# Performance work log

Hardware: AMD Instinct MI355X
Metric: run time of the kernel (lower is better)

The kernel has to match this reference:

```python
import jax, jax.numpy as jnp
import numpy as np

B, L, D, H = 4, 2048, 256, 512


def silu_backward(x):
    s = jax.nn.silu(x)
    return s + jax.nn.sigmoid(x) * (1.0 - s)


def setup_inputs() -> dict:
    key = jax.random.key(0)
    ks = jax.random.split(key, 12)
    sc = 0.02
    return {
        "x": jax.random.normal(ks[0], (B, L, D), jnp.float32),
        "W1": jax.random.normal(ks[1], (B, H, D), jnp.float32) * sc,
        "W2": jax.random.normal(ks[2], (B, D, H), jnp.float32) * sc,
        "Wq": jax.random.normal(ks[3], (D, D), jnp.float32) * sc,
        "bq": jnp.zeros((D,), jnp.float32),
        "Wk": jax.random.normal(ks[4], (D, D), jnp.float32) * sc,
        "bk": jnp.zeros((D,), jnp.float32),
        "Wv": jax.random.normal(ks[5], (D, D), jnp.float32) * sc,
        "bv": jnp.zeros((D,), jnp.float32),
        "w_lr": jax.random.normal(ks[6], (D,), jnp.float32) * sc,
        "b_lr": jnp.zeros((), jnp.float32),
        "w_wd": jax.random.normal(ks[7], (D,), jnp.float32) * sc,
        "b_wd": jnp.zeros((), jnp.float32),
        "log_base_lr": jnp.asarray(np.log(0.1), jnp.float32),
        "log_base_wd": jnp.asarray(np.log(0.5), jnp.float32),
    }


def reference(x, W1, W2, Wq, bq, Wk, bk, Wv, bv, w_lr, b_lr, w_wd, b_wd, log_base_lr, log_base_wd):
    b, l, d = x.shape
    query = x @ Wq + bq
    key = x @ Wk + bk
    value = x @ Wv + bv
    lr = jnp.exp(log_base_lr) * jax.nn.sigmoid(x @ w_lr + b_lr)          # [b,l]
    log_wd = jnp.log(1.0 - jnp.exp(log_base_wd) * jax.nn.sigmoid(x @ w_wd + b_wd))  # [b,l]

    wd_cross = jnp.exp(jnp.cumsum(log_wd, axis=1))                       # [b,l]
    idx = jnp.arange(l)
    strict_upper = idx[:, None] < idx[None, :]                           # (m, j): j > m
    A = jnp.where(strict_upper[None], log_wd[:, None, :], 0.0)           # [b,m,j]
    wd_inner = jnp.exp(jnp.cumsum(A, axis=2)) * (idx[:, None] <= idx[None, :])[None]  # [b,m,j]

    X1 = key
    Z1 = jnp.einsum('bhd,bld->blh', W1, X1)
    X2 = jax.nn.silu(Z1)
    Z2 = jnp.einsum('bdh,blh->bld', W2, X2)
    grad_Z2 = Z2 - value
    grad_X2 = jnp.einsum('bdh,bld->blh', W2, grad_Z2)
    grad_Z1 = silu_backward(Z1) * grad_X2

    X1_ = query
    mask_X1X1_ = jnp.einsum('bld,bmd->blm', X1, X1_) * wd_inner
    Z1_inner = -jnp.einsum('blh,bl,blm->bmh', grad_Z1, lr, mask_X1X1_)
    Z1_cross = jnp.einsum('bhd,bld,bl->blh', W1, X1_, wd_cross)
    Z1_ = Z1_inner + Z1_cross

    W1_next = (-jnp.einsum('blh,bl,bld->bhd', grad_Z1, lr * wd_inner[:, :, -1], X1)
               + W1 * wd_cross[:, -1][:, None, None])

    X2_ = jax.nn.silu(Z1_)
    mask_X2X2_ = jnp.einsum('blh,bmh->blm', X2, X2_) * wd_inner
    Z2_inner = -jnp.einsum('bld,bl,blm->bmd', grad_Z2, lr, mask_X2X2_)
    Z2_cross = jnp.einsum('bdh,blh,bl->bld', W2, X2_, wd_cross)
    Z2_ = Z2_inner + Z2_cross

    W2_next = (-jnp.einsum('bld,bl,blh->bdh', grad_Z2, lr * wd_inner[:, :, -1], X2)
               + W2 * wd_cross[:, -1][:, None, None])

    return (Z2_, W1_next, W2_next)
```

## Files before the change

### kernel.cpp

```cpp
#include <hip/hip_runtime.h>

typedef __bf16 bf16;
typedef __bf16 bf16x8 __attribute__((ext_vector_type(8)));
typedef __bf16 bf16x4 __attribute__((ext_vector_type(4)));
typedef float  f32x4  __attribute__((ext_vector_type(4)));

#define SB 72
#define SP 136
#define CUTOFF -25.0

__device__ __forceinline__ float silu_f(float x){
  float s = 1.f/(1.f+__expf(-x));
  return x*s;
}
__device__ __forceinline__ float silu_bwd_f(float x){
  float s = 1.f/(1.f+__expf(-x));
  float si = x*s;
  return si + s*(1.f-si);
}

struct MArgs {
  const bf16* A; const bf16* B;
  long sA, sB;
  int lda, ldb;
  int M, N, K;
  int mode;
  float* Cf; long sCf;
  bf16*  Cb; long sCb;
  bf16*  Cb2; long sCb2;
  bf16*  Ct;  long sCt;  int ldct;
  int ldc;
  const float* auxf; int ldax; long sAuxf;
  const bf16*  auxb; long sAuxb;
  const float* rowv; long sRowv;
  const double* cd;  long sCd;
  const float* ks;   long sKs;
  const float* clp;  long sClp;
  bf16* Q; bf16* Ko; float* Vo; const float* bqkv;
};

template<int TM>
__device__ __forceinline__ void gemm_body(const MArgs& g, int bm, int bn, int bz)
{
  const int row0 = bm*TM, col0 = bn*64;
  constexpr int NI  = TM/32;
  constexpr int TPR = 256/TM;
  constexpr int EPR = 64/TPR;
  constexpr int NCH = EPR/8;

  const bf16* A = g.A + (long)bz*g.sA;
  const bf16* B = g.B + (long)bz*g.sB;
  const float* ksp = g.ks ? g.ks + (long)bz*g.sKs : (const float*)0;
  const double* cd = g.cd ? g.cd + (long)bz*g.sCd : (const double*)0;
  float* Cf = g.Cf ? g.Cf + (long)bz*g.sCf : (float*)0;
  bf16* Cb  = g.Cb ? g.Cb + (long)bz*g.sCb : (bf16*)0;
  bf16* Cb2 = g.Cb2 ? g.Cb2 + (long)bz*g.sCb2 : (bf16*)0;
  bf16* Ct  = g.Ct ? g.Ct + (long)bz*g.sCt : (bf16*)0;
  const float* auxf = g.auxf ? g.auxf + (long)bz*g.sAuxf : (const float*)0;
  const bf16*  auxb = g.auxb ? g.auxb + (long)bz*g.sAuxb : (const bf16*)0;
  const float* rowv = g.rowv ? g.rowv + (long)bz*g.sRowv : (const float*)0;

  const int tid = threadIdx.x;
  const int mode = g.mode;
  const int lane = tid & 63;
  const int w = tid >> 6;
  const int wr = (w >> 1) * (TM/2), wc = (w & 1) * 32;
  const int l15 = lane & 15;
  const int quad = lane >> 4;

  __shared__ __align__(16) bf16 As[TM*SB];
  __shared__ __align__(16) bf16 Bs[64*SB];

  f32x4 acc[NI][2];
  #pragma unroll
  for (int i=0;i<NI;i++)
    #pragma unroll
    for (int j=0;j<2;j++)
      #pragma unroll
      for (int r=0;r<4;r++) acc[i][j][r] = 0.f;

  const int rowA = tid / TPR, kA = (tid % TPR) * EPR;
  const int rowB = tid >> 2,  kB = (tid & 3) * 16;

  int klo = 0;
  if (cd && ksp) {
    const double cref = cd[g.K-1];
    while (klo + 64 < g.K && (cref - cd[klo+63]) < CUTOFF) klo += 64;
  }

  for (int k0 = klo; k0 < g.K; k0 += 64) {
    {
      const bf16* s = A + (long)(row0+rowA)*g.lda + k0 + kA;
      bf16x8 v[NCH];
      #pragma unroll
      for (int p=0;p<NCH;p++) v[p] = *(const bf16x8*)(s + p*8);
      if (ksp) {
        #pragma unroll
        for (int p=0;p<NCH;p++)
          #pragma unroll
          for (int i=0;i<8;i++)
            v[p][i] = (bf16)((float)v[p][i] * ksp[k0+kA+p*8+i]);
      }
      #pragma unroll
      for (int p=0;p<NCH;p++) *(bf16x8*)&As[rowA*SB + kA + p*8] = v[p];
    }
    {
      const bf16* s = B + (long)(col0+rowB)*g.ldb + k0 + kB;
      *(bf16x8*)&Bs[rowB*SB + kB]     = *(const bf16x8*)s;
      *(bf16x8*)&Bs[rowB*SB + kB + 8] = *(const bf16x8*)(s+8);
    }
    __syncthreads();
    #pragma unroll
    for (int ch=0; ch<2; ch++){
      bf16x8 af[NI], bf2[2];
      #pragma unroll
      for (int i=0;i<NI;i++) af[i]  = *(const bf16x8*)&As[(wr + i*16 + l15)*SB + ch*32 + quad*8];
      #pragma unroll
      for (int j=0;j<2;j++) bf2[j] = *(const bf16x8*)&Bs[(wc + j*16 + l15)*SB + ch*32 + quad*8];
      #pragma unroll
      for (int i=0;i<NI;i++)
        #pragma unroll
        for (int j=0;j<2;j++)
          acc[i][j] = __builtin_amdgcn_mfma_f32_16x16x32_bf16(af[i], bf2[j], acc[i][j], 0, 0, 0);
    }
    __syncthreads();
  }

  float clv = 0.f;
  if (mode == 10) clv = *(g.clp + (long)bz*g.sClp);

  #pragma unroll
  for (int i=0;i<NI;i++){
    const int rb = row0 + wr + i*16 + quad*4;
    #pragma unroll
    for (int j=0;j<2;j++){
      const int c = col0 + wc + j*16 + l15;
      bf16 tv[4]; bool doT = false;
      #pragma unroll
      for (int reg=0; reg<4; reg++){
        const int r = rb + reg;
        float v = acc[i][j][reg];
        const long co = (long)r*g.ldc + c;
        switch (mode) {
          case 1: {
            Cb[co]  = (bf16)v;
            bf16 sv = (bf16)silu_f(v);
            Cb2[co] = sv;
            tv[reg] = sv; doT = true;
          } break;
          case 2: {
            bf16 o = (bf16)(v - auxf[(long)r*g.ldax + c]);
            Cb[co] = o; tv[reg] = o; doT = true;
          } break;
          case 3: {
            bf16 o = (bf16)(silu_bwd_f((float)auxb[(long)r*g.ldax + c]) * v * rowv[r]);
            Cb[co] = o; tv[reg] = o; doT = true;
          } break;
          case 10: {
            Cf[co] = v + auxf[(long)r*g.ldax + c]*clv;
          } break;
          case 11: {
            float o = v + g.bqkv[c];
            if (c < 256)      g.Q [(long)r*256 + c]       = (bf16)o;
            else if (c < 512) { g.Ko[(long)r*256 + (c-256)] = (bf16)o; tv[reg] = (bf16)o; doT = true; }
            else              g.Vo[(long)r*256 + (c-512)] = o;
          } break;
        }
      }
      if (doT && Ct) {
        bf16x4 t4 = { tv[0], tv[1], tv[2], tv[3] };
        if (mode == 11) {
          const int b = rb / g.ldct, l = rb % g.ldct;
          *(bf16x4*)&Ct[(long)b*g.sCt + (long)(c-256)*g.ldct + l] = t4;
        } else {
          *(bf16x4*)&Ct[(long)c*g.ldct + rb] = t4;
        }
      }
    }
  }
}

__global__ __launch_bounds__(256)
void mfma_gemm128(MArgs g){ gemm_body<128>(g, blockIdx.x, blockIdx.y, blockIdx.z); }

__global__ __launch_bounds__(256)
void mfma_gemm64(MArgs g){ gemm_body<64>(g, blockIdx.x, blockIdx.y, blockIdx.z); }

__global__ __launch_bounds__(256)
void wnext_gemm(MArgs g1, MArgs g2){
  const int z = blockIdx.z;
  const MArgs& g = (z < 4) ? g1 : g2;
  const int bz = z & 3;
  if ((int)blockIdx.x*128 >= g.M || (int)blockIdx.y*64 >= g.N) return;
  gemm_body<128>(g, blockIdx.x, blockIdx.y, bz);
}

struct FArgs {
  const bf16 *A, *B1, *B2, *W;
  long sA, sB1, sB2, sW;
  int ldb2;
  const double* cd; long sCd;
  const float* colv; long sColv;
  const float* wdc; long sWdc;
  float* Cf; long sCf;
  bf16* Cb; long sCb;
  int ldc;
};

template<int KS64, int ISF2, int ZSPLIT>
__global__ __launch_bounds__(256)
void fused_inner(FArgs g)
{
  const int m0 = blockIdx.x*64, n0 = blockIdx.y*128;
  const int bz   = ZSPLIT ? (blockIdx.z >> 1) : blockIdx.z;
  const int half = ZSPLIT ? (blockIdx.z & 1)  : 0;
  const int K1 = KS64*64;
  const bf16* A  = g.A  + (long)bz*g.sA;
  const bf16* B1 = g.B1 + (long)bz*g.sB1;
  const bf16* B2 = g.B2 + (long)bz*g.sB2;
  const bf16* W  = g.W  + (long)bz*g.sW;
  const double* cd = g.cd + (long)bz*g.sCd;
  const float* colv = ISF2 ? (g.colv + (long)bz*g.sColv) : (const float*)0;
  const float* wdc = g.wdc + (long)bz*g.sWdc;

  int lb = 0;
  while (lb + 128 <= m0 && (cd[m0] - cd[lb+127]) < CUTOFF) lb += 128;
  if (ZSPLIT && half == 1 && lb + 128 > m0) return;

  const int tid = threadIdx.x;
  const int lane = tid & 63, w = tid >> 6;
  const int wr = (w>>1)*32, wc = (w&1)*64;
  const int l15 = lane & 15, quad = lane >> 4;
  const int rowA = tid >> 2, kA = (tid & 3) * 16;
  const int rowB = tid >> 1, kB = (tid & 1) * 32;

  __shared__ __align__(16) bf16 As[64*SB];
  __shared__ __align__(16) bf16 Bs[128*SB];
  __shared__ __align__(16) bf16 Ps[64*SP];

  f32x4 O[2][4];
  #pragma unroll
  for (int i=0;i<2;i++)
    #pragma unroll
    for (int j=0;j<4;j++)
      #pragma unroll
      for (int r=0;r<4;r++) O[i][j][r] = 0.f;

  if (half == 0) {
    for (int ks=0; ks<KS64; ks++){
      const int k0 = ks*64;
      {
        const bf16* s = A + (long)(m0+rowA)*K1 + k0 + kA;
        *(bf16x8*)&As[rowA*SB + kA]     = *(const bf16x8*)s;
        *(bf16x8*)&As[rowA*SB + kA + 8] = *(const bf16x8*)(s+8);
      }
      {
        const bf16* s = W + (long)(n0+rowB)*K1 + k0 + kB;
        #pragma unroll
        for (int p=0;p<4;p++) *(bf16x8*)&Bs[rowB*SB + kB + p*8] = *(const bf16x8*)(s + p*8);
      }
      __syncthreads();
      #pragma unroll
      for (int ch=0; ch<2; ch++){
        bf16x8 af[2], bfr[4];
        #pragma unroll
        for (int i=0;i<2;i++) af[i]  = *(const bf16x8*)&As[(wr + i*16 + l15)*SB + ch*32 + quad*8];
        #pragma unroll
        for (int j=0;j<4;j++) bfr[j] = *(const bf16x8*)&Bs[(wc + j*16 + l15)*SB + ch*32 + quad*8];
        #pragma unroll
        for (int i=0;i<2;i++)
          #pragma unroll
          for (int j=0;j<4;j++)
            O[i][j] = __builtin_amdgcn_mfma_f32_16x16x32_bf16(af[i], bfr[j], O[i][j], 0, 0, 0);
      }
      __syncthreads();
    }
    #pragma unroll
    for (int i=0;i<2;i++)
      #pragma unroll
      for (int reg=0; reg<4; reg++){
        const float s = wdc[m0 + wr + i*16 + quad*4 + reg];
        #pragma unroll
        for (int j=0;j<4;j++) O[i][j][reg] *= s;
      }
  }

  const int lstep = ZSPLIT ? 256 : 128;
  for (int l0 = lb + half*128; l0 <= m0; l0 += lstep) {
    f32x4 P[2][4];
    #pragma unroll
    for (int i=0;i<2;i++)
      #pragma unroll
      for (int j=0;j<4;j++)
        #pragma unroll
        for (int r=0;r<4;r++) P[i][j][r] = 0.f;

    for (int ks=0; ks<KS64; ks++){
      const int k0 = ks*64;
      {
        const bf16* s = A + (long)(m0+rowA)*K1 + k0 + kA;
        *(bf16x8*)&As[rowA*SB + kA]     = *(const bf16x8*)s;
        *(bf16x8*)&As[rowA*SB + kA + 8] = *(const bf16x8*)(s+8);
      }
      {
        const bf16* s = B1 + (long)(l0+rowB)*K1 + k0 + kB;
        #pragma unroll
        for (int p=0;p<4;p++) *(bf16x8*)&Bs[rowB*SB + kB + p*8] = *(const bf16x8*)(s + p*8);
      }
      __syncthreads();
      #pragma unroll
      for (int ch=0; ch<2; ch++){
        bf16x8 af[2], bfr[4];
        #pragma unroll
        for (int i=0;i<2;i++) af[i]  = *(const bf16x8*)&As[(wr + i*16 + l15)*SB + ch*32 + quad*8];
        #pragma unroll
        for (int j=0;j<4;j++) bfr[j] = *(const bf16x8*)&Bs[(wc + j*16 + l15)*SB + ch*32 + quad*8];
        #pragma unroll
        for (int i=0;i<2;i++)
          #pragma unroll
          for (int j=0;j<4;j++)
            P[i][j] = __builtin_amdgcn_mfma_f32_16x16x32_bf16(af[i], bfr[j], P[i][j], 0, 0, 0);
      }
      __syncthreads();
    }

    {
      float cl[4], lrv[4];
      #pragma unroll
      for (int j=0;j<4;j++){
        const int l = l0 + wc + j*16 + l15;
        cl[j] = (float)cd[l];
        if (ISF2) lrv[j] = colv[l];
      }
      #pragma unroll
      for (int i=0;i<2;i++)
        #pragma unroll
        for (int reg=0; reg<4; reg++){
          const int mloc = wr + i*16 + quad*4 + reg;
          const int m = m0 + mloc;
          const float cm2 = (float)cd[m];
          #pragma unroll
          for (int j=0;j<4;j++){
            const int lloc = wc + j*16 + l15;
            const int l = l0 + lloc;
            float v = -P[i][j][reg] * __expf(cm2 - cl[j]);
            if (ISF2) v *= lrv[j];
            if (l > m) v = 0.f;
            Ps[mloc*SP + lloc] = (bf16)v;
          }
        }
    }
    __syncthreads();

    for (int st=0; st<2; st++){
      {
        const bf16* s = B2 + (long)(n0+rowB)*g.ldb2 + l0 + st*64 + kB;
        #pragma unroll
        for (int p=0;p<4;p++) *(bf16x8*)&Bs[rowB*SB + kB + p*8] = *(const bf16x8*)(s + p*8);
      }
      __syncthreads();
      #pragma unroll
      for (int ch=0; ch<2; ch++){
        bf16x8 af[2], bfr[4];
        #pragma unroll
        for (int i=0;i<2;i++) af[i]  = *(const bf16x8*)&Ps[(wr + i*16 + l15)*SP + st*64 + ch*32 + quad*8];
        #pragma unroll
        for (int j=0;j<4;j++) bfr[j] = *(const bf16x8*)&Bs[(wc + j*16 + l15)*SB + ch*32 + quad*8];
        #pragma unroll
        for (int i=0;i<2;i++)
          #pragma unroll
          for (int j=0;j<4;j++)
            O[i][j] = __builtin_amdgcn_mfma_f32_16x16x32_bf16(af[i], bfr[j], O[i][j], 0, 0, 0);
      }
      __syncthreads();
    }
  }

  #pragma unroll
  for (int i=0;i<2;i++){
    const int rb = m0 + wr + i*16 + quad*4;
    #pragma unroll
    for (int j=0;j<4;j++){
      const int c = n0 + wc + j*16 + l15;
      #pragma unroll
      for (int reg=0; reg<4; reg++){
        const long co = (long)(rb+reg)*g.ldc + c;
        if (ZSPLIT)     unsafeAtomicAdd(&g.Cf[(long)bz*g.sCf + co], O[i][j][reg]);
        else if (ISF2)  g.Cf[(long)bz*g.sCf + co] = O[i][j][reg];
        else            g.Cb[(long)bz*g.sCb + co] = (bf16)silu_f(O[i][j][reg]);
      }
    }
  }
}

__global__ __launch_bounds__(256)
void conv_multi(const float* __restrict__ a, bf16* __restrict__ oa, long na,
                const float* __restrict__ b, bf16* __restrict__ ob, long nb,
                const float* __restrict__ c, bf16* __restrict__ oc, long nc)
{
  const int job = blockIdx.y;
  const float* src = job==0 ? a : (job==1 ? b : c);
  bf16* dst       = job==0 ? oa : (job==1 ? ob : oc);
  const long n    = job==0 ? na : (job==1 ? nb : nc);
  long i = ((long)blockIdx.x*256 + threadIdx.x)*8;
  if (i >= n) return;
  float4 x = *(const float4*)&src[i];
  float4 y = *(const float4*)&src[i+4];
  bf16x8 o;
  o[0]=(bf16)x.x; o[1]=(bf16)x.y; o[2]=(bf16)x.z; o[3]=(bf16)x.w;
  o[4]=(bf16)y.x; o[5]=(bf16)y.y; o[6]=(bf16)y.z; o[7]=(bf16)y.w;
  *(bf16x8*)&dst[i] = o;
}

__global__ __launch_bounds__(256)
void transpose_qkv(const float* __restrict__ Wq, const float* __restrict__ Wk,
                   const float* __restrict__ Wv, bf16* __restrict__ out)
{
  __shared__ bf16 t[64][72];
  const int z = blockIdx.z;
  const float* ip = z==0 ? Wq : (z==1 ? Wk : Wv);
  bf16* op = out + (long)z*256*256;
  const int r0 = blockIdx.x*64, c0 = blockIdx.y*64;
  const int tid = threadIdx.x;
  const int lr_ = tid>>2, lc = (tid&3)*16;
  #pragma unroll
  for (int q=0;q<4;q++){
    float4 a = *(const float4*)&ip[(long)(r0+lr_)*256 + c0+lc + q*4];
    t[lr_][lc+q*4+0] = (bf16)a.x; t[lr_][lc+q*4+1] = (bf16)a.y;
    t[lr_][lc+q*4+2] = (bf16)a.z; t[lr_][lc+q*4+3] = (bf16)a.w;
  }
  __syncthreads();
  const int oc = tid>>2, orr = (tid&3)*16;
  bf16x8 u, v;
  #pragma unroll
  for (int i=0;i<8;i++){ u[i] = t[orr+i][oc]; v[i] = t[orr+8+i][oc]; }
  *(bf16x8*)&op[(long)(c0+oc)*256 + r0+orr]   = u;
  *(bf16x8*)&op[(long)(c0+oc)*256 + r0+orr+8] = v;
}

__global__ __launch_bounds__(256)
void transpose_f32_bf16(const float* __restrict__ in, bf16* __restrict__ out,
                        int R, int C, long sIn, long sOut)
{
  __shared__ bf16 t[64][72];
  const float* ip = in + (long)blockIdx.z*sIn;
  bf16* op = out + (long)blockIdx.z*sOut;
  const int r0 = blockIdx.x*64, c0 = blockIdx.y*64;
  const int tid = threadIdx.x;
  const int lr_ = tid>>2, lc = (tid&3)*16;
  #pragma unroll
  for (int q=0;q<4;q++){
    float4 a = *(const float4*)&ip[(long)(r0+lr_)*C + c0+lc + q*4];
    t[lr_][lc+q*4+0] = (bf16)a.x; t[lr_][lc+q*4+1] = (bf16)a.y;
    t[lr_][lc+q*4+2] = (bf16)a.z; t[lr_][lc+q*4+3] = (bf16)a.w;
  }
  __syncthreads();
  const int oc = tid>>2, orr = (tid&3)*16;
  bf16x8 u, v;
  #pragma unroll
  for (int i=0;i<8;i++){ u[i] = t[orr+i][oc]; v[i] = t[orr+8+i][oc]; }
  *(bf16x8*)&op[(long)(c0+oc)*R + r0+orr]   = u;
  *(bf16x8*)&op[(long)(c0+oc)*R + r0+orr+8] = v;
}

__global__ __launch_bounds__(256)
void scalar_proj_kernel(const float* __restrict__ x,
                        const float* __restrict__ wlr, const float* __restrict__ blr,
                        const float* __restrict__ wwd, const float* __restrict__ bwd,
                        const float* __restrict__ lbl, const float* __restrict__ lbw,
                        float* __restrict__ lr, float* __restrict__ lw)
{
  const int row  = blockIdx.x*4 + (threadIdx.x >> 6);
  const int lane = threadIdx.x & 63;
  const float4 a = ((const float4*)(x + (long)row*256))[lane];
  const float4 u = ((const float4*)wlr)[lane];
  const float4 w = ((const float4*)wwd)[lane];
  float d1 = a.x*u.x + a.y*u.y + a.z*u.z + a.w*u.w;
  float d2 = a.x*w.x + a.y*w.y + a.z*w.z + a.w*w.w;
  #pragma unroll
  for (int off=32; off; off>>=1) {
    d1 += __shfl_down(d1, off);
    d2 += __shfl_down(d2, off);
  }
  if (lane == 0) {
    float s1 = 1.f/(1.f+expf(-(d1 + blr[0])));
    lr[row] = expf(lbl[0]) * s1;
    float s2 = 1.f/(1.f+expf(-(d2 + bwd[0])));
    lw[row] = logf(1.f - expf(lbw[0]) * s2);
  }
}

__global__ __launch_bounds__(256)
void cumsum_kernel(const float* __restrict__ lw, const float* __restrict__ lr,
                   double* __restrict__ cd, float* __restrict__ wdc,
                   float* __restrict__ se1, float* __restrict__ se2, int L,
                   const float* __restrict__ bq, const float* __restrict__ bk,
                   const float* __restrict__ bv, float* __restrict__ bqkv)
{
  const int b = blockIdx.x;
  const int t = threadIdx.x;
  if (b == 4) {
    for (int i = t; i < 768; i += 256)
      bqkv[i] = (i<256) ? bq[i] : ((i<512) ? bk[i-256] : bv[i-512]);
    return;
  }
  const float* lwb = lw + (long)b*L;
  __shared__ double sum_s[256];
  double loc[8];
  double s = 0.0;
  #pragma unroll
  for (int i=0;i<8;i++){ s += (double)lwb[t*8+i]; loc[i] = s; }
  sum_s[t] = s;
  __syncthreads();
  for (int off=1; off<256; off<<=1){
    double v = 0.0;
    if (t >= off) v = sum_s[t-off];
    __syncthreads();
    sum_s[t] += v;
    __syncthreads();
  }
  const double prefix = (t > 0) ? sum_s[t-1] : 0.0;
  const double total  = sum_s[255];
  #pragma unroll
  for (int i=0;i<8;i++){
    double c = prefix + loc[i];
    long idx = (long)b*L + t*8 + i;
    cd[idx]  = c;
    wdc[idx] = (float)exp(c);
    double e = exp(total - c);
    se1[idx] = (float)(-e);
    se2[idx] = (float)(-e) * lr[idx];
  }
}

extern "C" void kernel_launch(void* const* d_in, const int* in_sizes, int n_in,
                              void* d_out, int out_size, void* d_ws, size_t ws_size,
                              hipStream_t stream)
{
  const int Bn = 4, L = 2048, D = 256, H = 512;
  const long LD = (long)L*D, LH = (long)L*H, HD = (long)H*D;

  const float* x   = (const float*)d_in[0];
  const float* W1  = (const float*)d_in[1];
  const float* W2  = (const float*)d_in[2];
  const float* Wq  = (const float*)d_in[3];
  const float* bq  = (const float*)d_in[4];
  const float* Wk  = (const float*)d_in[5];
  const float* bk  = (const float*)d_in[6];
  const float* Wv  = (const float*)d_in[7];
  const float* bv  = (const float*)d_in[8];
  const float* wlr = (const float*)d_in[9];
  const float* blr = (const float*)d_in[10];
  const float* wwd = (const float*)d_in[11];
  const float* bwd = (const float*)d_in[12];
  const float* lbl = (const float*)d_in[13];
  const float* lbw = (const float*)d_in[14];
  (void)in_sizes; (void)n_in; (void)out_size; (void)ws_size;

  float* out0 = (float*)d_out;
  float* out1 = out0 + (long)Bn*LD;
  float* out2 = out1 + (long)Bn*HD;

  char* wsp = (char*)d_ws;
  size_t off = 0;
  auto alloc = [&](size_t bytes)->void*{
    void* p = wsp + off; off += (bytes + 255) & ~(size_t)255; return p;
  };
  bf16* xb    = (bf16*)alloc((size_t)Bn*LD*2);
  bf16* Wqkvt = (bf16*)alloc((size_t)3*D*D*2);
  float* bqkv = (float*)alloc((size_t)3*D*4);
  bf16* W1b  = (bf16*)alloc((size_t)Bn*HD*2);
  bf16* W2b  = (bf16*)alloc((size_t)Bn*HD*2);
  bf16* W2t  = (bf16*)alloc((size_t)Bn*HD*2);
  bf16* Qb   = (bf16*)alloc((size_t)Bn*LD*2);
  bf16* Kb   = (bf16*)alloc((size_t)Bn*LD*2);
  bf16* Kt   = (bf16*)alloc((size_t)Bn*LD*2);
  float* Vf  = (float*)alloc((size_t)Bn*LD*4);
  bf16* Z1b  = (bf16*)alloc((size_t)Bn*LH*2);
  bf16* X2b  = (bf16*)alloc((size_t)Bn*LH*2);
  bf16* X2t  = (bf16*)alloc((size_t)Bn*LH*2);
  bf16* gZb  = (bf16*)alloc((size_t)Bn*LD*2);
  bf16* gZt  = (bf16*)alloc((size_t)Bn*LD*2);
  bf16* A1b  = (bf16*)alloc((size_t)Bn*LH*2);
  bf16* A1t  = (bf16*)alloc((size_t)Bn*LH*2);
  bf16* X2_b = (bf16*)alloc((size_t)Bn*LH*2);
  float* lrb = (float*)alloc((size_t)Bn*L*4);
  float* lwb = (float*)alloc((size_t)Bn*L*4);
  float* wdc = (float*)alloc((size_t)Bn*L*4);
  float* se1 = (float*)alloc((size_t)Bn*L*4);
  float* se2 = (float*)alloc((size_t)Bn*L*4);
  double* cdb = (double*)alloc((size_t)Bn*L*8);

  auto run128 = [&](const MArgs& g, int Z){
    dim3 grid(g.M/128, g.N/64, Z);
    mfma_gemm128<<<grid, 256, 0, stream>>>(g);
  };
  auto run64 = [&](const MArgs& g, int Z){
    dim3 grid(g.M/64, g.N/64, Z);
    mfma_gemm64<<<grid, 256, 0, stream>>>(g);
  };

  hipMemsetAsync(out0, 0, (size_t)Bn*LD*4, stream);

  conv_multi<<<dim3(1024,3), 256, 0, stream>>>(x, xb, Bn*LD, W1, W1b, Bn*HD, W2, W2b, Bn*HD);
  transpose_qkv<<<dim3(4,4,3), 256, 0, stream>>>(Wq, Wk, Wv, Wqkvt);
  transpose_f32_bf16<<<dim3(4,8,Bn), 256, 0, stream>>>(W2, W2t, D, H, HD, HD);
  scalar_proj_kernel<<<dim3(Bn*L/4), 256, 0, stream>>>(x, wlr, blr, wwd, bwd, lbl, lbw, lrb, lwb);
  cumsum_kernel<<<dim3(5), 256, 0, stream>>>(lwb, lrb, cdb, wdc, se1, se2, L, bq, bk, bv, bqkv);

  {
    MArgs g{}; g.A = xb; g.lda = D; g.B = Wqkvt; g.ldb = D;
    g.M = Bn*L; g.N = 3*D; g.K = D; g.mode = 11; g.ldc = 0;
    g.Q = Qb; g.Ko = Kb; g.Vo = Vf; g.bqkv = bqkv;
    g.Ct = Kt; g.sCt = LD; g.ldct = L;
    run128(g, 1);
  }
  {
    MArgs g{}; g.A = Kb; g.lda = D; g.sA = LD; g.B = W1b; g.ldb = D; g.sB = HD;
    g.M = L; g.N = H; g.K = D; g.mode = 1; g.ldc = H;
    g.Cb = Z1b; g.sCb = LH; g.Cb2 = X2b; g.sCb2 = LH;
    g.Ct = X2t; g.sCt = LH; g.ldct = L; run64(g, Bn);
  }
  {
    MArgs g{}; g.A = X2b; g.lda = H; g.sA = LH; g.B = W2b; g.ldb = H; g.sB = HD;
    g.M = L; g.N = D; g.K = H; g.mode = 2; g.ldc = D;
    g.auxf = Vf; g.ldax = D; g.sAuxf = LD; g.Cb = gZb; g.sCb = LD;
    g.Ct = gZt; g.sCt = LD; g.ldct = L; run64(g, Bn);
  }
  {
    MArgs g{}; g.A = gZb; g.lda = D; g.sA = LD; g.B = W2t; g.ldb = D; g.sB = HD;
    g.M = L; g.N = H; g.K = D; g.mode = 3; g.ldc = H;
    g.auxb = Z1b; g.ldax = H; g.sAuxb = LH; g.rowv = lrb; g.sRowv = L;
    g.Cb = A1b; g.sCb = LH;
    g.Ct = A1t; g.sCt = LH; g.ldct = L; run64(g, Bn);
  }
  {
    FArgs f{};
    f.A = Qb;  f.sA = LD;  f.B1 = Kb;  f.sB1 = LD;
    f.B2 = A1t; f.sB2 = LH; f.ldb2 = L;
    f.W = W1b; f.sW = HD;
    f.cd = cdb; f.sCd = L; f.wdc = wdc; f.sWdc = L;
    f.Cb = X2_b; f.sCb = LH; f.ldc = H;
    fused_inner<4,0,0><<<dim3(L/64, H/128, Bn), 256, 0, stream>>>(f);
  }
  {
    FArgs f{};
    f.A = X2_b; f.sA = LH; f.B1 = X2b; f.sB1 = LH;
    f.B2 = gZt; f.sB2 = LD; f.ldb2 = L;
    f.W = W2b; f.sW = HD;
    f.cd = cdb; f.sCd = L; f.colv = lrb; f.sColv = L; f.wdc = wdc; f.sWdc = L;
    f.Cf = out0; f.sCf = LD; f.ldc = D;
    fused_inner<8,1,1><<<dim3(L/64, D/128, Bn*2), 256, 0, stream>>>(f);
  }
  {
    MArgs g1{}; g1.A = A1t; g1.lda = L; g1.sA = LH; g1.B = Kt; g1.ldb = L; g1.sB = LD;
    g1.M = H; g1.N = D; g1.K = L; g1.mode = 10; g1.ldc = D;
    g1.ks = se1; g1.sKs = L; g1.cd = cdb; g1.sCd = L;
    g1.auxf = W1; g1.ldax = D; g1.sAuxf = HD; g1.clp = wdc + (L-1); g1.sClp = L;
    g1.Cf = out1; g1.sCf = HD;

    MArgs g2{}; g2.A = gZt; g2.lda = L; g2.sA = LD; g2.B = X2t; g2.ldb = L; g2.sB = LH;
    g2.M = D; g2.N = H; g2.K = L; g2.mode = 10; g2.ldc = H;
    g2.ks = se2; g2.sKs = L; g2.cd = cdb; g2.sCd = L;
    g2.auxf = W2; g2.ldax = H; g2.sAuxf = HD; g2.clp = wdc + (L-1); g2.sClp = L;
    g2.Cf = out2; g2.sCf = HD;

    wnext_gemm<<<dim3(4,8,8), 256, 0, stream>>>(g1, g2);
  }
}
```

Before: 251.0 us.

## Double K-tile depth to 128, swizzle fused-inner LDS, loosen decay cutoff, merge transposes

Raises the K step of the generic GEMM and the fused inner kernel from 64 to 128, so there are half as many barrier pairs per tile. In the fused kernel the padded LDS layout is replaced by an XOR swizzle, and the P@B2 stage now uses one 128-wide staging pass instead of two 64-wide ones. The decay cutoff for skipping negligible tiles is loosened from -25 to -18 so more K blocks are skipped, which adds approximation error. The two weight-transpose launches are merged into one kernel. LDS use per block grows, which may reduce occupancy.

```diff
diff --git a/kernel.cpp b/kernel.cpp
--- a/kernel.cpp
+++ b/kernel.cpp
@@ -5,9 +5,12 @@
 typedef __bf16 bf16x4 __attribute__((ext_vector_type(4)));
 typedef float  f32x4  __attribute__((ext_vector_type(4)));
 
-#define SB 72
-#define SP 136
-#define CUTOFF -25.0
+#define SB2 136
+#define CUTOFF -18.0
+
+__device__ __forceinline__ int swz(int r, int c){
+  return r*128 + ((((c>>3) ^ (r&15)) << 3) | (c & 7));
+}
 
 __device__ __forceinline__ float silu_f(float x){
   float s = 1.f/(1.f+__expf(-x));
@@ -44,8 +47,8 @@
 {
   const int row0 = bm*TM, col0 = bn*64;
   constexpr int NI  = TM/32;
-  constexpr int TPR = 256/TM;
-  constexpr int EPR = 64/TPR;
+  constexpr int TPR = 256/(TM);
+  constexpr int EPR = 128/TPR;
   constexpr int NCH = EPR/8;
 
   const bf16* A = g.A + (long)bz*g.sA;
@@ -68,8 +71,8 @@
   const int l15 = lane & 15;
   const int quad = lane >> 4;
 
-  __shared__ __align__(16) bf16 As[TM*SB];
-  __shared__ __align__(16) bf16 Bs[64*SB];
+  __shared__ __align__(16) bf16 As[TM*SB2];
+  __shared__ __align__(16) bf16 Bs[64*SB2];
 
   f32x4 acc[NI][2];
   #pragma unroll
@@ -80,15 +83,15 @@
       for (int r=0;r<4;r++) acc[i][j][r] = 0.f;
 
   const int rowA = tid / TPR, kA = (tid % TPR) * EPR;
-  const int rowB = tid >> 2,  kB = (tid & 3) * 16;
+  const int rowB = tid >> 2,  kB = (tid & 3) * 32;
 
   int klo = 0;
   if (cd && ksp) {
     const double cref = cd[g.K-1];
-    while (klo + 64 < g.K && (cref - cd[klo+63]) < CUTOFF) klo += 64;
-  }
-
-  for (int k0 = klo; k0 < g.K; k0 += 64) {
+    while (klo + 128 < g.K && (cref - cd[klo+127]) < CUTOFF) klo += 128;
+  }
+
+  for (int k0 = klo; k0 < g.K; k0 += 128) {
     {
       const bf16* s = A + (long)(row0+rowA)*g.lda + k0 + kA;
       bf16x8 v[NCH];
@@ -102,21 +105,21 @@
             v[p][i] = (bf16)((float)v[p][i] * ksp[k0+kA+p*8+i]);
       }
       #pragma unroll
-      for (int p=0;p<NCH;p++) *(bf16x8*)&As[rowA*SB + kA + p*8] = v[p];
+      for (int p=0;p<NCH;p++) *(bf16x8*)&As[rowA*SB2 + kA + p*8] = v[p];
     }
     {
       const bf16* s = B + (long)(col0+rowB)*g.ldb + k0 + kB;
-      *(bf16x8*)&Bs[rowB*SB + kB]     = *(const bf16x8*)s;
-      *(bf16x8*)&Bs[rowB*SB + kB + 8] = *(const bf16x8*)(s+8);
+      #pragma unroll
+      for (int p=0;p<4;p++) *(bf16x8*)&Bs[rowB*SB2 + kB + p*8] = *(const bf16x8*)(s + p*8);
     }
     __syncthreads();
     #pragma unroll
-    for (int ch=0; ch<2; ch++){
+    for (int ch=0; ch<4; ch++){
       bf16x8 af[NI], bf2[2];
       #pragma unroll
-      for (int i=0;i<NI;i++) af[i]  = *(const bf16x8*)&As[(wr + i*16 + l15)*SB + ch*32 + quad*8];
-      #pragma unroll
-      for (int j=0;j<2;j++) bf2[j] = *(const bf16x8*)&Bs[(wc + j*16 + l15)*SB + ch*32 + quad*8];
+      for (int i=0;i<NI;i++) af[i]  = *(const bf16x8*)&As[(wr + i*16 + l15)*SB2 + ch*32 + quad*8];
+      #pragma unroll
+      for (int j=0;j<2;j++) bf2[j] = *(const bf16x8*)&Bs[(wc + j*16 + l15)*SB2 + ch*32 + quad*8];
       #pragma unroll
       for (int i=0;i<NI;i++)
         #pragma unroll
@@ -207,14 +210,14 @@
   int ldc;
 };
 
-template<int KS64, int ISF2, int ZSPLIT>
+template<int KS128, int ISF2, int ZSPLIT>
 __global__ __launch_bounds__(256)
 void fused_inner(FArgs g)
 {
   const int m0 = blockIdx.x*64, n0 = blockIdx.y*128;
   const int bz   = ZSPLIT ? (blockIdx.z >> 1) : blockIdx.z;
   const int half = ZSPLIT ? (blockIdx.z & 1)  : 0;
-  const int K1 = KS64*64;
+  const int K1 = KS128*128;
   const bf16* A  = g.A  + (long)bz*g.sA;
   const bf16* B1 = g.B1 + (long)bz*g.sB1;
   const bf16* B2 = g.B2 + (long)bz*g.sB2;
@@ -231,12 +234,12 @@
   const int lane = tid & 63, w = tid >> 6;
   const int wr = (w>>1)*32, wc = (w&1)*64;
   const int l15 = lane & 15, quad = lane >> 4;
-  const int rowA = tid >> 2, kA = (tid & 3) * 16;
-  const int rowB = tid >> 1, kB = (tid & 1) * 32;
-
-  __shared__ __align__(16) bf16 As[64*SB];
-  __shared__ __align__(16) bf16 Bs[128*SB];
-  __shared__ __align__(16) bf16 Ps[64*SP];
+  const int rowA = tid >> 2, kA = (tid & 3) * 32;
+  const int rowB = tid >> 1, kB = (tid & 1) * 64;
+
+  __shared__ __align__(16) bf16 As[64*128];
+  __shared__ __align__(16) bf16 Bs[128*128];
+  __shared__ __align__(16) bf16 Ps[64*128];
 
   f32x4 O[2][4];
   #pragma unroll
@@ -246,27 +249,31 @@
       #pragma unroll
       for (int r=0;r<4;r++) O[i][j][r] = 0.f;
 
+  auto stageA = [&](int k0){
+    const bf16* s = A + (long)(m0+rowA)*K1 + k0 + kA;
+    #pragma unroll
+    for (int p=0;p<4;p++)
+      *(bf16x8*)&As[swz(rowA, kA + p*8)] = *(const bf16x8*)(s + p*8);
+  };
+  auto stageB = [&](const bf16* P, int ld, int rbase, int k0){
+    const bf16* s = P + (long)(rbase+rowB)*ld + k0 + kB;
+    #pragma unroll
+    for (int p=0;p<8;p++)
+      *(bf16x8*)&Bs[swz(rowB, kB + p*8)] = *(const bf16x8*)(s + p*8);
+  };
+
   if (half == 0) {
-    for (int ks=0; ks<KS64; ks++){
-      const int k0 = ks*64;
-      {
-        const bf16* s = A + (long)(m0+rowA)*K1 + k0 + kA;
-        *(bf16x8*)&As[rowA*SB + kA]     = *(const bf16x8*)s;
-        *(bf16x8*)&As[rowA*SB + kA + 8] = *(const bf16x8*)(s+8);
-      }
-      {
-        const bf16* s = W + (long)(n0+rowB)*K1 + k0 + kB;
-        #pragma unroll
-        for (int p=0;p<4;p++) *(bf16x8*)&Bs[rowB*SB + kB + p*8] = *(const bf16x8*)(s + p*8);
-      }
+    for (int ks=0; ks<KS128; ks++){
+      stageA(ks*128);
+      stageB(W, K1, n0, ks*128);
       __syncthreads();
       #pragma unroll
-      for (int ch=0; ch<2; ch++){
+      for (int ch=0; ch<4; ch++){
         bf16x8 af[2], bfr[4];
         #pragma unroll
-        for (int i=0;i<2;i++) af[i]  = *(const bf16x8*)&As[(wr + i*16 + l15)*SB + ch*32 + quad*8];
-        #pragma unroll
-        for (int j=0;j<4;j++) bfr[j] = *(const bf16x8*)&Bs[(wc + j*16 + l15)*SB + ch*32 + quad*8];
+        for (int i=0;i<2;i++) af[i]  = *(const bf16x8*)&As[swz(wr + i*16 + l15, ch*32 + quad*8)];
+        #pragma unroll
+        for (int j=0;j<4;j++) bfr[j] = *(const bf16x8*)&Bs[swz(wc + j*16 + l15, ch*32 + quad*8)];
         #pragma unroll
         for (int i=0;i<2;i++)
           #pragma unroll
@@ -295,26 +302,17 @@
         #pragma unroll
         for (int r=0;r<4;r++) P[i][j][r] = 0.f;
 
-    for (int ks=0; ks<KS64; ks++){
-      const int k0 = ks*64;
-      {
-        const bf16* s = A + (long)(m0+rowA)*K1 + k0 + kA;
-        *(bf16x8*)&As[rowA*SB + kA]     = *(const bf16x8*)s;
-        *(bf16x8*)&As[rowA*SB + kA + 8] = *(const bf16x8*)(s+8);
-      }
-      {
-        const bf16* s = B1 + (long)(l0+rowB)*K1 + k0 + kB;
-        #pragma unroll
-        for (int p=0;p<4;p++) *(bf16x8*)&Bs[rowB*SB + kB + p*8] = *(const bf16x8*)(s + p*8);
-      }
+    for (int ks=0; ks<KS128; ks++){
+      stageA(ks*128);
+      stageB(B1, K1, l0, ks*128);
       __syncthreads();
       #pragma unroll
-      for (int ch=0; ch<2; ch++){
+      for (int ch=0; ch<4; ch++){
         bf16x8 af[2], bfr[4];
         #pragma unroll
-        for (int i=0;i<2;i++) af[i]  = *(const bf16x8*)&As[(wr + i*16 + l15)*SB + ch*32 + quad*8];
-        #pragma unroll
-        for (int j=0;j<4;j++) bfr[j] = *(const bf16x8*)&Bs[(wc + j*16 + l15)*SB + ch*32 + quad*8];
+        for (int i=0;i<2;i++) af[i]  = *(const bf16x8*)&As[swz(wr + i*16 + l15, ch*32 + quad*8)];
+        #pragma unroll
+        for (int j=0;j<4;j++) bfr[j] = *(const bf16x8*)&Bs[swz(wc + j*16 + l15, ch*32 + quad*8)];
         #pragma unroll
         for (int i=0;i<2;i++)
           #pragma unroll
@@ -346,34 +344,27 @@
             float v = -P[i][j][reg] * __expf(cm2 - cl[j]);
             if (ISF2) v *= lrv[j];
             if (l > m) v = 0.f;
-            Ps[mloc*SP + lloc] = (bf16)v;
+            Ps[swz(mloc, lloc)] = (bf16)v;
           }
         }
     }
+    stageB(B2, g.ldb2, n0, l0);
     __syncthreads();
 
-    for (int st=0; st<2; st++){
-      {
-        const bf16* s = B2 + (long)(n0+rowB)*g.ldb2 + l0 + st*64 + kB;
-        #pragma unroll
-        for (int p=0;p<4;p++) *(bf16x8*)&Bs[rowB*SB + kB + p*8] = *(const bf16x8*)(s + p*8);
-      }
-      __syncthreads();
-      #pragma unroll
-      for (int ch=0; ch<2; ch++){
-        bf16x8 af[2], bfr[4];
-        #pragma unroll
-        for (int i=0;i<2;i++) af[i]  = *(const bf16x8*)&Ps[(wr + i*16 + l15)*SP + st*64 + ch*32 + quad*8];
-        #pragma unroll
-        for (int j=0;j<4;j++) bfr[j] = *(const bf16x8*)&Bs[(wc + j*16 + l15)*SB + ch*32 + quad*8];
-        #pragma unroll
-        for (int i=0;i<2;i++)
-          #pragma unroll
-          for (int j=0;j<4;j++)
-            O[i][j] = __builtin_amdgcn_mfma_f32_16x16x32_bf16(af[i], bfr[j], O[i][j], 0, 0, 0);
-      }
-      __syncthreads();
-    }
+    #pragma unroll
+    for (int ch=0; ch<4; ch++){
+      bf16x8 af[2], bfr[4];
+      #pragma unroll
+      for (int i=0;i<2;i++) af[i]  = *(const bf16x8*)&Ps[swz(wr + i*16 + l15, ch*32 + quad*8)];
+      #pragma unroll
+      for (int j=0;j<4;j++) bfr[j] = *(const bf16x8*)&Bs[swz(wc + j*16 + l15, ch*32 + quad*8)];
+      #pragma unroll
+      for (int i=0;i<2;i++)
+        #pragma unroll
+        for (int j=0;j<4;j++)
+          O[i][j] = __builtin_amdgcn_mfma_f32_16x16x32_bf16(af[i], bfr[j], O[i][j], 0, 0, 0);
+    }
+    __syncthreads();
   }
 
   #pragma unroll
@@ -413,38 +404,23 @@
 }
 
 __global__ __launch_bounds__(256)
-void transpose_qkv(const float* __restrict__ Wq, const float* __restrict__ Wk,
-                   const float* __restrict__ Wv, bf16* __restrict__ out)
+void transpose_multi(const float* __restrict__ Wq, const float* __restrict__ Wk,
+                     const float* __restrict__ Wv, bf16* __restrict__ Wqkvt,
+                     const float* __restrict__ W2, bf16* __restrict__ W2t, long HD)
 {
   __shared__ bf16 t[64][72];
   const int z = blockIdx.z;
-  const float* ip = z==0 ? Wq : (z==1 ? Wk : Wv);
-  bf16* op = out + (long)z*256*256;
-  const int r0 = blockIdx.x*64, c0 = blockIdx.y*64;
-  const int tid = threadIdx.x;
-  const int lr_ = tid>>2, lc = (tid&3)*16;
-  #pragma unroll
-  for (int q=0;q<4;q++){
-    float4 a = *(const float4*)&ip[(long)(r0+lr_)*256 + c0+lc + q*4];
-    t[lr_][lc+q*4+0] = (bf16)a.x; t[lr_][lc+q*4+1] = (bf16)a.y;
-    t[lr_][lc+q*4+2] = (bf16)a.z; t[lr_][lc+q*4+3] = (bf16)a.w;
-  }
-  __syncthreads();
-  const int oc = tid>>2, orr = (tid&3)*16;
-  bf16x8 u, v;
-  #pragma unroll
-  for (int i=0;i<8;i++){ u[i] = t[orr+i][oc]; v[i] = t[orr+8+i][oc]; }
-  *(bf16x8*)&op[(long)(c0+oc)*256 + r0+orr]   = u;
-  *(bf16x8*)&op[(long)(c0+oc)*256 + r0+orr+8] = v;
-}
-
-__global__ __launch_bounds__(256)
-void transpose_f32_bf16(const float* __restrict__ in, bf16* __restrict__ out,
-                        int R, int C, long sIn, long sOut)
-{
-  __shared__ bf16 t[64][72];
-  const float* ip = in + (long)blockIdx.z*sIn;
-  bf16* op = out + (long)blockIdx.z*sOut;
+  const float* ip; bf16* op; int R, C;
+  if (z < 3) {
+    if (blockIdx.y >= 4) return;
+    ip = z==0 ? Wq : (z==1 ? Wk : Wv);
+    op = Wqkvt + (long)z*256*256;
+    R = 256; C = 256;
+  } else {
+    ip = W2 + (long)(z-3)*HD;
+    op = W2t + (long)(z-3)*HD;
+    R = 256; C = 512;
+  }
   const int r0 = blockIdx.x*64, c0 = blockIdx.y*64;
   const int tid = threadIdx.x;
   const int lr_ = tid>>2, lc = (tid&3)*16;
@@ -603,8 +579,7 @@
   hipMemsetAsync(out0, 0, (size_t)Bn*LD*4, stream);
 
   conv_multi<<<dim3(1024,3), 256, 0, stream>>>(x, xb, Bn*LD, W1, W1b, Bn*HD, W2, W2b, Bn*HD);
-  transpose_qkv<<<dim3(4,4,3), 256, 0, stream>>>(Wq, Wk, Wv, Wqkvt);
-  transpose_f32_bf16<<<dim3(4,8,Bn), 256, 0, stream>>>(W2, W2t, D, H, HD, HD);
+  transpose_multi<<<dim3(4,8,7), 256, 0, stream>>>(Wq, Wk, Wv, Wqkvt, W2, W2t, HD);
   scalar_proj_kernel<<<dim3(Bn*L/4), 256, 0, stream>>>(x, wlr, blr, wwd, bwd, lbl, lbw, lrb, lwb);
   cumsum_kernel<<<dim3(5), 256, 0, stream>>>(lwb, lrb, cdb, wdc, se1, se2, L, bq, bk, bv, bqkv);
 
@@ -641,7 +616,7 @@
     f.W = W1b; f.sW = HD;
     f.cd = cdb; f.sCd = L; f.wdc = wdc; f.sWdc = L;
     f.Cb = X2_b; f.sCb = LH; f.ldc = H;
-    fused_inner<4,0,0><<<dim3(L/64, H/128, Bn), 256, 0, stream>>>(f);
+    fused_inner<2,0,0><<<dim3(L/64, H/128, Bn), 256, 0, stream>>>(f);
   }
   {
     FArgs f{};
@@ -650,7 +625,7 @@
     f.W = W2b; f.sW = HD;
     f.cd = cdb; f.sCd = L; f.colv = lrb; f.sColv = L; f.wdc = wdc; f.sWdc = L;
     f.Cf = out0; f.sCf = LD; f.ldc = D;
-    fused_inner<8,1,1><<<dim3(L/64, D/128, Bn*2), 256, 0, stream>>>(f);
+    fused_inner<4,1,1><<<dim3(L/64, D/128, Bn*2), 256, 0, stream>>>(f);
   }
   {
     MArgs g1{}; g1.A = A1t; g1.lda = L; g1.sA = LH; g1.B = Kt; g1.ldb = L; g1.sB = LD;
```

Result: slower. 286.4 us (+14.1%).
